# Kernel tuning notes

Measured on AMD Instinct MI355X. Metric: run time of the kernel, lower is better.

The kernel has to match this reference:

```python
import jax, jax.numpy as jnp
import numpy as np

B, S, IN, H, NC, WSEG = 2, 256, 80, 128, 40, 64
F2 = 2 * H  # bidirectional LSTM output dim


def setup_inputs() -> dict:
    key = jax.random.key(0)
    it = iter(jax.random.split(key, 48))
    def nrm(shape, scale):
        return jax.random.normal(next(it), shape, jnp.float32) * scale
    d = {}
    d["x"] = jax.random.normal(next(it), (B, S, IN), jnp.float32)
    d["lengths"] = jnp.full((B,), S, dtype=jnp.int32)
    ins = [IN, F2]
    for l in range(2):
        for dr in ("f", "b"):
            sc = 1.0 / np.sqrt(H)
            d[f"w_ih_l{l}{dr}"] = nrm((4 * H, ins[l]), sc)
            d[f"w_hh_l{l}{dr}"] = nrm((4 * H, H), sc)
            d[f"b_l{l}{dr}"] = nrm((4 * H,), sc)
    PD = 3 * F2  # pairwise phi feature dim
    d["a_s0"] = jnp.float32(0.25); d["w_s1"] = nrm((100, PD), 1.0 / np.sqrt(PD)); d["b_s1"] = jnp.zeros((100,), jnp.float32)
    d["a_s1"] = jnp.float32(0.25); d["w_s2"] = nrm((1, 100), 0.1); d["b_s2"] = jnp.zeros((1,), jnp.float32)
    d["a_c0"] = jnp.float32(0.25); d["w_c1"] = nrm((2 * NC, F2), 1.0 / np.sqrt(F2)); d["b_c1"] = jnp.zeros((2 * NC,), jnp.float32)
    d["a_c1"] = jnp.float32(0.25); d["w_c2"] = nrm((NC, 2 * NC), 0.1); d["b_c2"] = jnp.zeros((NC,), jnp.float32)
    d["a_b0"] = jnp.float32(0.25); d["w_b1"] = nrm((2 * NC, F2), 1.0 / np.sqrt(F2)); d["b_b1"] = jnp.zeros((2 * NC,), jnp.float32)
    d["a_b1"] = jnp.float32(0.25); d["w_b2"] = nrm((2, 2 * NC), 0.1); d["b_b2"] = jnp.zeros((2,), jnp.float32)
    return d


def prelu(x, a):
    return jnp.where(x >= 0, x, a * x)


def mlp(x, a0, W1, b1, a1, W2, b2):
    h = prelu(x, a0) @ W1.T + b1
    return prelu(h, a1) @ W2.T + b2


def lstm_dir(x, Wih, Whh, b, reverse):
    # PyTorch gate order: i, f, g, o
    pre = jnp.einsum("bsi,gi->sbg", x, Wih) + b  # [S,B,4H]
    if reverse:
        pre = pre[::-1]
    h0 = jnp.zeros((x.shape[0], Whh.shape[1]), x.dtype)
    def step(carry, xt):
        h, c = carry
        g = xt + h @ Whh.T
        i, f, gg, o = jnp.split(g, 4, axis=-1)
        c = jax.nn.sigmoid(f) * c + jax.nn.sigmoid(i) * jnp.tanh(gg)
        h = jax.nn.sigmoid(o) * jnp.tanh(c)
        return (h, c), h
    _, hs = jax.lax.scan(step, (h0, h0), pre)
    if reverse:
        hs = hs[::-1]
    return jnp.swapaxes(hs, 0, 1)  # [B,S,H]


def encode(x, layers):
    out = x
    for (wif, whf, bf, wib, whb, bb) in layers:
        out = jnp.concatenate([
            lstm_dir(out, wif, whf, bf, False),
            lstm_dir(out, wib, whb, bb, True),
        ], axis=-1)
    return out


def compute_scores(rnn_out, a_s0, w_s1, b_s1, a_s1, w_s2, b_s2):
    cum = jnp.cumsum(rnn_out, axis=1)
    # phi[b,i,j] = [cum[j]-cum[i], out[i], out[j]]  (faithful to calc_phi)
    c = cum[:, None, :, :] - cum[:, :, None, :]
    sh = c.shape
    dmat = jnp.broadcast_to(rnn_out[:, :, None, :], sh)
    emat = jnp.broadcast_to(rnn_out[:, None, :, :], sh)
    phi = jnp.concatenate([c, dmat, emat], axis=-1)  # [B,S,S,3*F2]
    return mlp(phi, a_s0, w_s1, b_s1, a_s1, w_s2, b_s2)[..., 0]  # [B,S,S]


def dp_backptr(scores):
    # Viterbi-style DP: best[i] = max_{j in [i-WSEG, i)} best[j] + scores[:, j, i]
    Bn, Sn = scores.shape[:2]
    def step(best, i):
        start = jnp.maximum(0, i - WSEG)
        jidx = start + jnp.arange(WSEG)
        bwin = jax.lax.dynamic_slice(best, (0, start), (Bn, WSEG))
        swin = jax.lax.dynamic_slice(scores, (0, start, i), (Bn, WSEG, 1))[..., 0]
        cand = jnp.where(jidx[None, :] < i, bwin + swin, -1e9)
        k = (start + jnp.argmax(cand, axis=1)).astype(jnp.int32)
        best = jax.lax.dynamic_update_slice(best, jnp.max(cand, axis=1, keepdims=True), (0, i))
        return best, k
    _, ks = jax.lax.scan(step, jnp.zeros((Bn, Sn), scores.dtype), jnp.arange(1, Sn))
    backptr = jnp.concatenate([jnp.zeros((1, Bn), jnp.int32), ks], axis=0).T  # [B,S]
    return backptr


def backtrack(scores, backptr, lengths):
    Bn, Sn = scores.shape[:2]
    bar = jnp.arange(Bn)
    def step(carry, _):
        cur, acc, bm = carry
        bm = bm.at[bar, cur].set(True)
        prev = backptr[bar, cur]
        active = cur > 0
        acc = acc + jnp.where(active, scores[bar, prev, cur], 0.0)
        cur = jnp.where(active, prev, 0)
        return (cur, acc, bm), None
    init = ((lengths - 1).astype(jnp.int32), jnp.zeros((Bn,), scores.dtype), jnp.zeros((Bn, Sn), bool))
    (_, acc, bm), _ = jax.lax.scan(step, init, None, length=Sn)
    return bm, acc


def reference(x, lengths,
              w_ih_l0f, w_hh_l0f, b_l0f, w_ih_l0b, w_hh_l0b, b_l0b,
              w_ih_l1f, w_hh_l1f, b_l1f, w_ih_l1b, w_hh_l1b, b_l1b,
              a_s0, w_s1, b_s1, a_s1, w_s2, b_s2,
              a_c0, w_c1, b_c1, a_c1, w_c2, b_c2,
              a_b0, w_b1, b_b1, a_b1, w_b2, b_b2):
    layers = [
        (w_ih_l0f, w_hh_l0f, b_l0f, w_ih_l0b, w_hh_l0b, b_l0b),
        (w_ih_l1f, w_hh_l1f, b_l1f, w_ih_l1b, w_hh_l1b, b_l1b),
    ]
    rnn_out = encode(x, layers)  # [B,S,2H]
    cls_out = mlp(rnn_out, a_c0, w_c1, b_c1, a_c1, w_c2, b_c2)
    bin_out = mlp(rnn_out, a_b0, w_b1, b_b1, a_b1, w_b2, b_b2)
    scores = compute_scores(rnn_out, a_s0, w_s1, b_s1, a_s1, w_s2, b_s2)
    backptr = dp_backptr(scores)
    bmask, pred_scores = backtrack(scores, backptr, lengths)
    # bmask[b,i]==1 iff i is a predicted segment boundary (padded-dense encoding of pred lists)
    return cls_out, bin_out, bmask.astype(jnp.int32), pred_scores
```

## Files before the change

kernel.cpp:

```cpp
#include <hip/hip_runtime.h>
#include <math.h>


#define OFF_BIN 20480
#define OFF_BM  21504
#define OFF_PRED 22016

__device__ __forceinline__ float preluf(float x, float a) { return x >= 0.f ? x : a * x; }
__device__ __forceinline__ float sigf(float x) { return 1.f / (1.f + __expf(-x)); }
__device__ __forceinline__ float tanh_fast(float x) { return 1.f - 2.f / (__expf(2.f * x) + 1.f); }

__global__ __launch_bounds__(256) void k_gemm(const float* __restrict__ A,
                                              const float* __restrict__ B,
                                              int Adim, int K,
                                              const float* __restrict__ wf,
                                              const float* __restrict__ bf,
                                              const float* __restrict__ wb,
                                              const float* __restrict__ bbv,
                                              float* __restrict__ outF,
                                              float* __restrict__ outB) {
    int mtile = blockIdx.y;
    int dir = mtile >> 3;
    const float* W = dir ? wb : wf;
    const float* bias = dir ? bbv : bf;
    float* out = dir ? outB : outF;
    int g0 = (mtile & 7) << 6;
    int tb0 = blockIdx.x << 6;
    int tid = threadIdx.x;
    int Bdim = K - Adim;

    __shared__ float Ws[16][68];
    __shared__ float Xs[16][68];

    int r = tid >> 2, c4 = tid & 3;
    int tbr = tb0 + r;
    int hr = ((tbr & 1) << 8) | (tbr >> 1);
    int ty = tid >> 4;
    int tx = tid & 15;
    float acc[4][4] = {};

    for (int k0 = 0; k0 < K; k0 += 16) {
        float4 wv = *(const float4*)(W + (size_t)(g0 + r) * K + k0 + (c4 << 2));
        const float* src = (k0 < Adim) ? (A + (size_t)hr * Adim + k0)
                                       : (B + (size_t)hr * Bdim + (k0 - Adim));
        float4 xv = *(const float4*)(src + (c4 << 2));
        __syncthreads();
        int kc = c4 << 2;
        Ws[kc + 0][r] = wv.x; Ws[kc + 1][r] = wv.y; Ws[kc + 2][r] = wv.z; Ws[kc + 3][r] = wv.w;
        Xs[kc + 0][r] = xv.x; Xs[kc + 1][r] = xv.y; Xs[kc + 2][r] = xv.z; Xs[kc + 3][r] = xv.w;
        __syncthreads();
#pragma unroll
        for (int kk = 0; kk < 16; ++kk) {
            float4 wq = *(const float4*)&Ws[kk][ty << 2];
            float4 xq = *(const float4*)&Xs[kk][tx << 2];
            acc[0][0] += wq.x * xq.x; acc[0][1] += wq.x * xq.y; acc[0][2] += wq.x * xq.z; acc[0][3] += wq.x * xq.w;
            acc[1][0] += wq.y * xq.x; acc[1][1] += wq.y * xq.y; acc[1][2] += wq.y * xq.z; acc[1][3] += wq.y * xq.w;
            acc[2][0] += wq.z * xq.x; acc[2][1] += wq.z * xq.y; acc[2][2] += wq.z * xq.z; acc[2][3] += wq.z * xq.w;
            acc[3][0] += wq.w * xq.x; acc[3][1] += wq.w * xq.y; acc[3][2] += wq.w * xq.z; acc[3][3] += wq.w * xq.w;
        }
    }
    int gq = g0 + (ty << 2);
    float b0 = bias[gq], b1 = bias[gq + 1], b2 = bias[gq + 2], b3 = bias[gq + 3];
#pragma unroll
    for (int j = 0; j < 4; ++j) {
        int tb = tb0 + (tx << 2) + j;
        float4 v = make_float4(acc[0][j] + b0, acc[1][j] + b1, acc[2][j] + b2, acc[3][j] + b3);
        *(float4*)(out + (size_t)tb * 512 + gq) = v;
    }
}

__global__ __launch_bounds__(512, 2) void k_lstm(const float* __restrict__ pre_f,
                                                 const float* __restrict__ pre_b,
                                                 const float* __restrict__ whh_f,
                                                 const float* __restrict__ whh_b,
                                                 float* __restrict__ hout_f,
                                                 float* __restrict__ hout_b) {
    const int dir = blockIdx.x >> 1;
    const int b = blockIdx.x & 1;
    const float* pre = dir ? pre_b : pre_f;
    const float* whh = dir ? whh_b : whh_f;
    float* hout = dir ? hout_b : hout_f;
    const int tid = threadIdx.x;
    const int c = tid >> 7;
    const int gg = tid & 127;
    const int k0 = c << 5;

    float w[4][32];
#pragma unroll
    for (int j = 0; j < 4; ++j) {
#pragma unroll
        for (int k = 0; k < 32; k += 4) {
            float4 v = *(const float4*)(whh + (size_t)((j << 7) + gg) * 128 + k0 + k);
            w[j][k] = v.x; w[j][k + 1] = v.y; w[j][k + 2] = v.z; w[j][k + 3] = v.w;
        }
    }

    __shared__ __align__(16) float hl[128];
    __shared__ float4 part[4][128];
    if (tid < 128) hl[tid] = 0.f;
    float cst = 0.f;
    __syncthreads();

    int t0 = dir ? 255 : 0;
    const float* pp0 = pre + ((size_t)t0 * 2 + b) * 512;
    float p0 = pp0[gg], p1 = pp0[128 + gg], p2 = pp0[256 + gg], p3 = pp0[384 + gg];

    for (int step = 0; step < 256; ++step) {
        int t = dir ? (255 - step) : step;
        float n0 = 0.f, n1 = 0.f, n2 = 0.f, n3 = 0.f;
        if (step < 255) {
            int tn = dir ? (254 - step) : (step + 1);
            const float* pp = pre + ((size_t)tn * 2 + b) * 512;
            n0 = pp[gg]; n1 = pp[128 + gg]; n2 = pp[256 + gg]; n3 = pp[384 + gg];
        }
        float a0 = 0.f, a1 = 0.f, a2 = 0.f, a3 = 0.f;
#pragma unroll
        for (int k = 0; k < 32; k += 4) {
            float4 h4 = *(const float4*)(hl + k0 + k);
            a0 += w[0][k] * h4.x + w[0][k + 1] * h4.y + w[0][k + 2] * h4.z + w[0][k + 3] * h4.w;
            a1 += w[1][k] * h4.x + w[1][k + 1] * h4.y + w[1][k + 2] * h4.z + w[1][k + 3] * h4.w;
            a2 += w[2][k] * h4.x + w[2][k + 1] * h4.y + w[2][k + 2] * h4.z + w[2][k + 3] * h4.w;
            a3 += w[3][k] * h4.x + w[3][k + 1] * h4.y + w[3][k + 2] * h4.z + w[3][k + 3] * h4.w;
        }
        part[c][gg] = make_float4(a0, a1, a2, a3);
        __syncthreads();
        float4 q0 = part[0][gg], q1 = part[1][gg], q2 = part[2][gg], q3 = part[3][gg];
        float gi = p0 + ((q0.x + q1.x) + (q2.x + q3.x));
        float gf = p1 + ((q0.y + q1.y) + (q2.y + q3.y));
        float gG = p2 + ((q0.z + q1.z) + (q2.z + q3.z));
        float go = p3 + ((q0.w + q1.w) + (q2.w + q3.w));
        cst = sigf(gf) * cst + sigf(gi) * tanh_fast(gG);
        float h = sigf(go) * tanh_fast(cst);
        hl[gg] = h;
        if (tid < 128) hout[(size_t)(((b << 8) + t) << 7) + gg] = h;
        p0 = n0; p1 = n1; p2 = n2; p3 = n3;
        __syncthreads();
    }
}

__global__ __launch_bounds__(256) void k_feats(const float* __restrict__ h1f,
                                               const float* __restrict__ h1b,
                                               const float* __restrict__ ws1,
                                               const float* __restrict__ bs1,
                                               const float* a_s0,
                                               float* __restrict__ Pd,
                                               float* __restrict__ Pe,
                                               const float* ac0p, const float* __restrict__ wc1,
                                               const float* __restrict__ bc1, const float* ac1p,
                                               const float* __restrict__ wc2, const float* __restrict__ bc2,
                                               const float* ab0p, const float* __restrict__ wb1,
                                               const float* __restrict__ bb1, const float* ab1p,
                                               const float* __restrict__ wb2, const float* __restrict__ bb2,
                                               float* __restrict__ out,
                                               float* __restrict__ cum) {
    __shared__ __align__(16) float xa[256];
    __shared__ __align__(16) float xb2[256];
    __shared__ __align__(16) float hc[80];
    __shared__ __align__(16) float hb[80];
    int bid = blockIdx.x;
    int tid = threadIdx.x;
    int kk = tid & 127;
    if (bid < 512) {
        int row = bid;
        float a0 = a_s0[0];
        float v = ((tid < 128) ? h1f : h1b)[(size_t)row * 128 + kk];
        xa[tid] = preluf(v, a0);
        __syncthreads();
        const float4* p4 = (const float4*)xa;
        if (tid < 100) {
            const float4* wr = (const float4*)(ws1 + (size_t)tid * 768 + 256);
            float acc = bs1[tid];
#pragma unroll 8
            for (int q = 0; q < 64; ++q) {
                float4 w4 = wr[q], x4 = p4[q];
                acc += w4.x * x4.x + w4.y * x4.y + w4.z * x4.z + w4.w * x4.w;
            }
            Pd[(size_t)row * 100 + tid] = acc;
        } else if (tid >= 128 && tid < 228) {
            int u = tid - 128;
            const float4* wr = (const float4*)(ws1 + (size_t)u * 768 + 512);
            float acc = 0.f;
#pragma unroll 8
            for (int q = 0; q < 64; ++q) {
                float4 w4 = wr[q], x4 = p4[q];
                acc += w4.x * x4.x + w4.y * x4.y + w4.z * x4.z + w4.w * x4.w;
            }
            Pe[(size_t)row * 100 + u] = acc;
        }
    } else if (bid < 1024) {
        int row = bid - 512;
        float ac0 = ac0p[0], ac1 = ac1p[0], ab0 = ab0p[0], ab1 = ab1p[0];
        float v = ((tid < 128) ? h1f : h1b)[(size_t)row * 128 + kk];
        xa[tid] = preluf(v, ac0);
        xb2[tid] = preluf(v, ab0);
        __syncthreads();
        if (tid < 80) {
            const float4* wr = (const float4*)(wc1 + (size_t)tid * 256);
            const float4* x4 = (const float4*)xa;
            float acc = bc1[tid];
#pragma unroll 8
            for (int q = 0; q < 64; ++q) {
                float4 w4 = wr[q], p = x4[q];
                acc += w4.x * p.x + w4.y * p.y + w4.z * p.z + w4.w * p.w;
            }
            hc[tid] = preluf(acc, ac1);
        } else if (tid >= 128 && tid < 208) {
            int u = tid - 128;
            const float4* wr = (const float4*)(wb1 + (size_t)u * 256);
            const float4* x4 = (const float4*)xb2;
            float acc = bb1[u];
#pragma unroll 8
            for (int q = 0; q < 64; ++q) {
                float4 w4 = wr[q], p = x4[q];
                acc += w4.x * p.x + w4.y * p.y + w4.z * p.z + w4.w * p.w;
            }
            hb[u] = preluf(acc, ab1);
        }
        __syncthreads();
        if (tid < 40) {
            const float4* wr = (const float4*)(wc2 + (size_t)tid * 80);
            const float4* h4 = (const float4*)hc;
            float acc = bc2[tid];
#pragma unroll
            for (int q = 0; q < 20; ++q) {
                float4 w4 = wr[q], p = h4[q];
                acc += w4.x * p.x + w4.y * p.y + w4.z * p.z + w4.w * p.w;
            }
            out[(size_t)row * 40 + tid] = acc;
        } else if (tid >= 64 && tid < 66) {
            int j = tid - 64;
            const float4* wr = (const float4*)(wb2 + (size_t)j * 80);
            const float4* h4 = (const float4*)hb;
            float acc = bb2[j];
#pragma unroll
            for (int q = 0; q < 20; ++q) {
                float4 w4 = wr[q], p = h4[q];
                acc += w4.x * p.x + w4.y * p.y + w4.z * p.z + w4.w * p.w;
            }
            out[OFF_BIN + (size_t)row * 2 + j] = acc;
        }
    } else {
        int b = bid - 1024;
        const float* src = (tid < 128) ? h1f : h1b;
        float run = 0.f;
#pragma unroll 8
        for (int t = 0; t < 256; ++t) {
            float v = src[(size_t)(((b << 8) + t) << 7) + kk];
            cum[(size_t)(((b << 8) + t) << 8) + tid] = run + v;
            run += v;
        }
    }
}

__global__ __launch_bounds__(256, 4) void k_scores(const float* __restrict__ cum,
                                                   const float* __restrict__ ws1,
                                                   const float* __restrict__ ws2,
                                                   const float* __restrict__ bs2,
                                                   const float* __restrict__ Pd,
                                                   const float* __restrict__ Pe,
                                                   const float* a_s0p, const float* a_s1p,
                                                   float* __restrict__ scT) {
    int bid = blockIdx.x;
    int dt = bid & 7, et = (bid >> 3) & 63, b = bid >> 9;
    int d0 = dt << 5, e0 = et << 2;
    int tid = threadIdx.x;
    __shared__ float cumd[32][257];
    __shared__ float cume[4][257];
    __shared__ float red[4][4][32];
    float a0 = a_s0p[0], a1 = a_s1p[0];

    {
        int r = tid & 31, w = tid >> 5;
        const float4* src = (const float4*)(cum + (size_t)(((b << 8) + (d0 + r)) << 8) + (w << 5));
        float* dst = &cumd[r][w << 5];
#pragma unroll
        for (int x = 0; x < 8; ++x) {
            float4 v = src[x];
            dst[(x << 2) + 0] = v.x; dst[(x << 2) + 1] = v.y;
            dst[(x << 2) + 2] = v.z; dst[(x << 2) + 3] = v.w;
        }
    }
    {
        int er = tid >> 6, j = tid & 63;
        float4 v = *((const float4*)(cum + (size_t)(((b << 8) + (e0 + er)) << 8)) + j);
        float* dst = &cume[er][j << 2];
        dst[0] = v.x; dst[1] = v.y; dst[2] = v.z; dst[3] = v.w;
    }
    __syncthreads();

    int ug = __builtin_amdgcn_readfirstlane(tid >> 6);
    int lane = tid & 63;
    int dd = lane & 31;
    int eh = lane >> 5;
    int ea = (eh << 1), ebn = ea + 1;
    float acc0[25], acc1[25];
#pragma unroll
    for (int t = 0; t < 25; ++t) { acc0[t] = 0.f; acc1[t] = 0.f; }
    const float* wc = ws1 + (size_t)(ug * 25) * 768;

    for (int k = 0; k < 256; k += 4) {
        float cd0 = cumd[dd][k], cd1 = cumd[dd][k + 1], cd2 = cumd[dd][k + 2], cd3 = cumd[dd][k + 3];
        float4 ya = make_float4(preluf(cume[ea][k] - cd0, a0), preluf(cume[ea][k + 1] - cd1, a0),
                                preluf(cume[ea][k + 2] - cd2, a0), preluf(cume[ea][k + 3] - cd3, a0));
        float4 yb = make_float4(preluf(cume[ebn][k] - cd0, a0), preluf(cume[ebn][k + 1] - cd1, a0),
                                preluf(cume[ebn][k + 2] - cd2, a0), preluf(cume[ebn][k + 3] - cd3, a0));
#pragma unroll
        for (int t = 0; t < 25; ++t) {
            float4 wq = *(const float4*)(wc + (size_t)t * 768 + k);
            acc0[t] += ya.x * wq.x + ya.y * wq.y + ya.z * wq.z + ya.w * wq.w;
            acc1[t] += yb.x * wq.x + yb.y * wq.y + yb.z * wq.z + yb.w * wq.w;
        }
    }

    const float* pdrow = Pd + (size_t)((b << 8) + d0 + dd) * 100;
    {
        const float* perow = Pe + (size_t)((b << 8) + e0 + ea) * 100;
        float part = 0.f;
#pragma unroll
        for (int t = 0; t < 25; ++t) {
            int u = ug * 25 + t;
            float h = acc0[t] + pdrow[u] + perow[u];
            part += preluf(h, a1) * ws2[u];
        }
        red[ug][ea][dd] = part;
    }
    {
        const float* perow = Pe + (size_t)((b << 8) + e0 + ebn) * 100;
        float part = 0.f;
#pragma unroll
        for (int t = 0; t < 25; ++t) {
            int u = ug * 25 + t;
            float h = acc1[t] + pdrow[u] + perow[u];
            part += preluf(h, a1) * ws2[u];
        }
        red[ug][ebn][dd] = part;
    }
    __syncthreads();
    if (tid < 128) {
        int e = tid >> 5, l2 = tid & 31;
        float s = red[0][e][l2] + red[1][e][l2] + red[2][e][l2] + red[3][e][l2] + bs2[0];
        scT[(size_t)(((b << 8) + (e0 + e)) << 8) + d0 + l2] = s;
    }
}

__device__ __forceinline__ void argmax_dpp(float& v, int& ki) {
#define AD_STEP(CTRL, RMASK)                                                                    \
    {                                                                                           \
        int mv = __builtin_amdgcn_update_dpp(__float_as_int(v), __float_as_int(v), CTRL, RMASK, 0xf, false); \
        int mk = __builtin_amdgcn_update_dpp(ki, ki, CTRL, RMASK, 0xf, false);                  \
        float fv = __int_as_float(mv);                                                          \
        bool take = (fv > v) || (fv == v && mk < ki);                                           \
        v = take ? fv : v;                                                                      \
        ki = take ? mk : ki;                                                                    \
    }
    AD_STEP(0x111, 0xf)
    AD_STEP(0x112, 0xf)
    AD_STEP(0x114, 0xf)
    AD_STEP(0x118, 0xf)
    AD_STEP(0x142, 0xa)
    AD_STEP(0x143, 0xc)
#undef AD_STEP
}

__global__ __launch_bounds__(128) void k_dp(const float* __restrict__ scT,
                                            const int* __restrict__ lengths,
                                            float* __restrict__ out) {
    __shared__ int bp[2][256];
    __shared__ float bm[2][256];
    int tid = threadIdx.x;
    for (int i = tid; i < 512; i += 128) {
        ((int*)bp)[i] = 0;
        ((float*)bm)[i] = 0.f;
    }
    __syncthreads();
    int b = tid >> 6, ln = tid & 63;
    const float* sb = scT + ((size_t)b << 16);
    int lenm1 = lengths[b] - 1;
    float wreg = 0.f;
    float bestFinal = 0.f;
    int jcur = (ln < 1) ? ln : ln - 64;
    float sc_next = sb[(1 << 8) + ((jcur < 0) ? 0 : jcur)];
    for (int i = 1; i < 256; ++i) {
        float sc = sc_next;
        int j = jcur;
        if (i < 255) {
            int m2 = (i + 1) & 63;
            int base2 = (i + 1) - m2;
            int j2 = (ln < m2) ? (base2 + ln) : (base2 + ln - 64);
            jcur = j2;
            sc_next = sb[((i + 1) << 8) + ((j2 < 0) ? 0 : j2)];
        }
        float v = (j >= 0) ? (wreg + sc) : -1000000000.0f;
        int ki = j;
        argmax_dpp(v, ki);
        float bv = __uint_as_float(__builtin_amdgcn_readlane(__float_as_uint(v), 63));
        int bk = __builtin_amdgcn_readlane(ki, 63);
        if (ln == (i & 63)) wreg = bv;
        if (ln == 0) bp[b][i] = bk;
        if (i == lenm1) bestFinal = bv;
    }
    if (ln == 0) out[OFF_PRED + b] = bestFinal;
    __syncthreads();
    if (tid < 2) {
        int bb = tid;
        int cur = lengths[bb] - 1;
        for (int it = 0; it < 256; ++it) {
            bm[bb][cur] = 1.f;
            int prev = bp[bb][cur];
            cur = (cur > 0) ? prev : 0;
        }
    }
    __syncthreads();
    for (int i = tid; i < 512; i += 128) out[OFF_BM + i] = ((float*)bm)[i];
}

extern "C" void kernel_launch(void* const* d_in, const int* in_sizes, int n_in,
                              void* d_out, int out_size, void* d_ws, size_t ws_size,
                              hipStream_t stream) {
    const float* x     = (const float*)d_in[0];
    const int* lengths = (const int*)d_in[1];
    const float* wih0f = (const float*)d_in[2];
    const float* whh0f = (const float*)d_in[3];
    const float* b0f   = (const float*)d_in[4];
    const float* wih0b = (const float*)d_in[5];
    const float* whh0b = (const float*)d_in[6];
    const float* b0b   = (const float*)d_in[7];
    const float* wih1f = (const float*)d_in[8];
    const float* whh1f = (const float*)d_in[9];
    const float* b1f   = (const float*)d_in[10];
    const float* wih1b = (const float*)d_in[11];
    const float* whh1b = (const float*)d_in[12];
    const float* b1b   = (const float*)d_in[13];
    const float* a_s0  = (const float*)d_in[14];
    const float* w_s1  = (const float*)d_in[15];
    const float* b_s1  = (const float*)d_in[16];
    const float* a_s1  = (const float*)d_in[17];
    const float* w_s2  = (const float*)d_in[18];
    const float* b_s2  = (const float*)d_in[19];
    const float* a_c0  = (const float*)d_in[20];
    const float* w_c1  = (const float*)d_in[21];
    const float* b_c1  = (const float*)d_in[22];
    const float* a_c1  = (const float*)d_in[23];
    const float* w_c2  = (const float*)d_in[24];
    const float* b_c2  = (const float*)d_in[25];
    const float* a_b0  = (const float*)d_in[26];
    const float* w_b1  = (const float*)d_in[27];
    const float* b_b1  = (const float*)d_in[28];
    const float* a_b1  = (const float*)d_in[29];
    const float* w_b2  = (const float*)d_in[30];
    const float* b_b2  = (const float*)d_in[31];

    float* wsf = (float*)d_ws;
    float* preF = wsf;
    float* preB = wsf + 262144;
    float* h0f  = wsf + 524288;
    float* h0b  = wsf + 589824;
    float* h1f  = wsf + 655360;
    float* h1b  = wsf + 720896;
    float* cum  = wsf + 786432;
    float* Pd   = wsf + 917504;
    float* Pe   = wsf + 968704;
    float* scT  = wsf + 1019904;
    float* out  = (float*)d_out;

    k_gemm<<<dim3(8, 16), 256, 0, stream>>>(x, x, 80, 80, wih0f, b0f, wih0b, b0b, preF, preB);
    k_lstm<<<4, 512, 0, stream>>>(preF, preB, whh0f, whh0b, h0f, h0b);
    k_gemm<<<dim3(8, 16), 256, 0, stream>>>(h0f, h0b, 128, 256, wih1f, b1f, wih1b, b1b, preF, preB);
    k_lstm<<<4, 512, 0, stream>>>(preF, preB, whh1f, whh1b, h1f, h1b);
    k_feats<<<1026, 256, 0, stream>>>(h1f, h1b, w_s1, b_s1, a_s0, Pd, Pe,
                                      a_c0, w_c1, b_c1, a_c1, w_c2, b_c2,
                                      a_b0, w_b1, b_b1, a_b1, w_b2, b_b2, out, cum);
    k_scores<<<1024, 256, 0, stream>>>(cum, w_s1, w_s2, b_s2, Pd, Pe, a_s0, a_s1, scT);
    k_dp<<<1, 128, 0, stream>>>(scT, lengths, out);
}
```

Baseline: 957.5 us.

## Batch LSTM preactivation loads and output stores; retile pairwise scores kernel

The LSTM recurrence now loads pre-activations for eight timesteps at once and buffers eight hidden outputs before writing them. This takes a global load off the serial per-step critical path. The dot product is split into two accumulator chains to shorten the dependency. The scores kernel is retiled to 512-thread blocks covering 64 d-rows and 4 e-rows, staging the cumulative sums in two K-halves so shared memory stays small while each weight load is reused across more rows. The costs are extra register pressure in both kernels, fewer blocks in the scores launch, and an extra barrier per K-half.

```diff
diff --git a/kernel.cpp b/kernel.cpp
--- a/kernel.cpp
+++ b/kernel.cpp
@@ -99,42 +99,60 @@
     __shared__ float4 part[4][128];
     if (tid < 128) hl[tid] = 0.f;
     float cst = 0.f;
+    float pf0[8], pf1[8], pf2[8], pf3[8], hb8[8];
     __syncthreads();
 
-    int t0 = dir ? 255 : 0;
-    const float* pp0 = pre + ((size_t)t0 * 2 + b) * 512;
-    float p0 = pp0[gg], p1 = pp0[128 + gg], p2 = pp0[256 + gg], p3 = pp0[384 + gg];
-
-    for (int step = 0; step < 256; ++step) {
-        int t = dir ? (255 - step) : step;
-        float n0 = 0.f, n1 = 0.f, n2 = 0.f, n3 = 0.f;
-        if (step < 255) {
-            int tn = dir ? (254 - step) : (step + 1);
-            const float* pp = pre + ((size_t)tn * 2 + b) * 512;
-            n0 = pp[gg]; n1 = pp[128 + gg]; n2 = pp[256 + gg]; n3 = pp[384 + gg];
-        }
-        float a0 = 0.f, a1 = 0.f, a2 = 0.f, a3 = 0.f;
-#pragma unroll
-        for (int k = 0; k < 32; k += 4) {
-            float4 h4 = *(const float4*)(hl + k0 + k);
-            a0 += w[0][k] * h4.x + w[0][k + 1] * h4.y + w[0][k + 2] * h4.z + w[0][k + 3] * h4.w;
-            a1 += w[1][k] * h4.x + w[1][k + 1] * h4.y + w[1][k + 2] * h4.z + w[1][k + 3] * h4.w;
-            a2 += w[2][k] * h4.x + w[2][k + 1] * h4.y + w[2][k + 2] * h4.z + w[2][k + 3] * h4.w;
-            a3 += w[3][k] * h4.x + w[3][k + 1] * h4.y + w[3][k + 2] * h4.z + w[3][k + 3] * h4.w;
-        }
-        part[c][gg] = make_float4(a0, a1, a2, a3);
-        __syncthreads();
-        float4 q0 = part[0][gg], q1 = part[1][gg], q2 = part[2][gg], q3 = part[3][gg];
-        float gi = p0 + ((q0.x + q1.x) + (q2.x + q3.x));
-        float gf = p1 + ((q0.y + q1.y) + (q2.y + q3.y));
-        float gG = p2 + ((q0.z + q1.z) + (q2.z + q3.z));
-        float go = p3 + ((q0.w + q1.w) + (q2.w + q3.w));
-        cst = sigf(gf) * cst + sigf(gi) * tanh_fast(gG);
-        float h = sigf(go) * tanh_fast(cst);
-        hl[gg] = h;
-        if (tid < 128) hout[(size_t)(((b << 8) + t) << 7) + gg] = h;
-        p0 = n0; p1 = n1; p2 = n2; p3 = n3;
-        __syncthreads();
+    for (int blk = 0; blk < 32; ++blk) {
+        if (tid < 128) {
+#pragma unroll
+            for (int s = 0; s < 8; ++s) {
+                int step = (blk << 3) + s;
+                int t = dir ? (255 - step) : step;
+                const float* pp = pre + ((size_t)t * 2 + b) * 512;
+                pf0[s] = pp[gg]; pf1[s] = pp[128 + gg];
+                pf2[s] = pp[256 + gg]; pf3[s] = pp[384 + gg];
+            }
+        }
+#pragma unroll
+        for (int s = 0; s < 8; ++s) {
+            float a0 = 0.f, a1 = 0.f, a2 = 0.f, a3 = 0.f;
+            float e0 = 0.f, e1 = 0.f, e2 = 0.f, e3 = 0.f;
+#pragma unroll
+            for (int k = 0; k < 32; k += 8) {
+                float4 hA = *(const float4*)(hl + k0 + k);
+                float4 hB = *(const float4*)(hl + k0 + k + 4);
+                a0 += w[0][k] * hA.x + w[0][k + 1] * hA.y + w[0][k + 2] * hA.z + w[0][k + 3] * hA.w;
+                e0 += w[0][k + 4] * hB.x + w[0][k + 5] * hB.y + w[0][k + 6] * hB.z + w[0][k + 7] * hB.w;
+                a1 += w[1][k] * hA.x + w[1][k + 1] * hA.y + w[1][k + 2] * hA.z + w[1][k + 3] * hA.w;
+                e1 += w[1][k + 4] * hB.x + w[1][k + 5] * hB.y + w[1][k + 6] * hB.z + w[1][k + 7] * hB.w;
+                a2 += w[2][k] * hA.x + w[2][k + 1] * hA.y + w[2][k + 2] * hA.z + w[2][k + 3] * hA.w;
+                e2 += w[2][k + 4] * hB.x + w[2][k + 5] * hB.y + w[2][k + 6] * hB.z + w[2][k + 7] * hB.w;
+                a3 += w[3][k] * hA.x + w[3][k + 1] * hA.y + w[3][k + 2] * hA.z + w[3][k + 3] * hA.w;
+                e3 += w[3][k + 4] * hB.x + w[3][k + 5] * hB.y + w[3][k + 6] * hB.z + w[3][k + 7] * hB.w;
+            }
+            part[c][gg] = make_float4(a0 + e0, a1 + e1, a2 + e2, a3 + e3);
+            __syncthreads();
+            if (tid < 128) {
+                float4 q0 = part[0][gg], q1 = part[1][gg], q2 = part[2][gg], q3 = part[3][gg];
+                float gi = pf0[s] + ((q0.x + q1.x) + (q2.x + q3.x));
+                float gf = pf1[s] + ((q0.y + q1.y) + (q2.y + q3.y));
+                float gG = pf2[s] + ((q0.z + q1.z) + (q2.z + q3.z));
+                float go = pf3[s] + ((q0.w + q1.w) + (q2.w + q3.w));
+                cst = sigf(gf) * cst + sigf(gi) * tanh_fast(gG);
+                float h = sigf(go) * tanh_fast(cst);
+                hl[gg] = h;
+                hb8[s] = h;
+            }
+            __syncthreads();
+        }
+        if (tid < 128) {
+            int base = blk << 3;
+#pragma unroll
+            for (int s = 0; s < 8; ++s) {
+                int t = dir ? (255 - (base + s)) : (base + s);
+                hout[(size_t)(((b << 8) + t) << 7) + gg] = hb8[s];
+            }
+        }
     }
 }
 
@@ -252,7 +270,7 @@
     }
 }
 
-__global__ __launch_bounds__(256, 4) void k_scores(const float* __restrict__ cum,
+__global__ __launch_bounds__(512, 2) void k_scores(const float* __restrict__ cum,
                                                    const float* __restrict__ ws1,
                                                    const float* __restrict__ ws2,
                                                    const float* __restrict__ bs2,
@@ -261,54 +279,59 @@
                                                    const float* a_s0p, const float* a_s1p,
                                                    float* __restrict__ scT) {
     int bid = blockIdx.x;
-    int dt = bid & 7, et = (bid >> 3) & 63, b = bid >> 9;
-    int d0 = dt << 5, e0 = et << 2;
+    int dt = bid & 3, et = (bid >> 2) & 63, b = bid >> 8;
+    int d0 = dt << 6, e0 = et << 2;
     int tid = threadIdx.x;
-    __shared__ float cumd[32][257];
-    __shared__ float cume[4][257];
-    __shared__ float red[4][4][32];
+    __shared__ float cumdh[64][129];
+    __shared__ float cumeh[4][129];
+    __shared__ float red[4][4][64];
     float a0 = a_s0p[0], a1 = a_s1p[0];
 
-    {
-        int r = tid & 31, w = tid >> 5;
-        const float4* src = (const float4*)(cum + (size_t)(((b << 8) + (d0 + r)) << 8) + (w << 5));
-        float* dst = &cumd[r][w << 5];
-#pragma unroll
-        for (int x = 0; x < 8; ++x) {
-            float4 v = src[x];
-            dst[(x << 2) + 0] = v.x; dst[(x << 2) + 1] = v.y;
-            dst[(x << 2) + 2] = v.z; dst[(x << 2) + 3] = v.w;
-        }
-    }
-    {
-        int er = tid >> 6, j = tid & 63;
-        float4 v = *((const float4*)(cum + (size_t)(((b << 8) + (e0 + er)) << 8)) + j);
-        float* dst = &cume[er][j << 2];
-        dst[0] = v.x; dst[1] = v.y; dst[2] = v.z; dst[3] = v.w;
-    }
-    __syncthreads();
-
-    int ug = __builtin_amdgcn_readfirstlane(tid >> 6);
-    int lane = tid & 63;
-    int dd = lane & 31;
-    int eh = lane >> 5;
-    int ea = (eh << 1), ebn = ea + 1;
+    int wv = tid >> 6;
+    int ug = __builtin_amdgcn_readfirstlane(wv & 3);
+    int eh = __builtin_amdgcn_readfirstlane(wv >> 2);
+    int dd = tid & 63;
+    int ea = eh << 1, ebn = ea + 1;
     float acc0[25], acc1[25];
 #pragma unroll
     for (int t = 0; t < 25; ++t) { acc0[t] = 0.f; acc1[t] = 0.f; }
     const float* wc = ws1 + (size_t)(ug * 25) * 768;
 
-    for (int k = 0; k < 256; k += 4) {
-        float cd0 = cumd[dd][k], cd1 = cumd[dd][k + 1], cd2 = cumd[dd][k + 2], cd3 = cumd[dd][k + 3];
-        float4 ya = make_float4(preluf(cume[ea][k] - cd0, a0), preluf(cume[ea][k + 1] - cd1, a0),
-                                preluf(cume[ea][k + 2] - cd2, a0), preluf(cume[ea][k + 3] - cd3, a0));
-        float4 yb = make_float4(preluf(cume[ebn][k] - cd0, a0), preluf(cume[ebn][k + 1] - cd1, a0),
-                                preluf(cume[ebn][k + 2] - cd2, a0), preluf(cume[ebn][k + 3] - cd3, a0));
-#pragma unroll
-        for (int t = 0; t < 25; ++t) {
-            float4 wq = *(const float4*)(wc + (size_t)t * 768 + k);
-            acc0[t] += ya.x * wq.x + ya.y * wq.y + ya.z * wq.z + ya.w * wq.w;
-            acc1[t] += yb.x * wq.x + yb.y * wq.y + yb.z * wq.z + yb.w * wq.w;
+    for (int half = 0; half < 2; ++half) {
+        int hk = half << 7;
+        __syncthreads();
+        {
+            int r = tid & 63, wq = tid >> 6;
+            const float4* src = (const float4*)(cum + (size_t)(((b << 8) + (d0 + r)) << 8) + hk + (wq << 4));
+            float* dst = &cumdh[r][wq << 4];
+#pragma unroll
+            for (int x = 0; x < 4; ++x) {
+                float4 v = src[x];
+                dst[(x << 2) + 0] = v.x; dst[(x << 2) + 1] = v.y;
+                dst[(x << 2) + 2] = v.z; dst[(x << 2) + 3] = v.w;
+            }
+        }
+        if (tid < 128) {
+            int er = tid >> 5, j = tid & 31;
+            float4 v = *((const float4*)(cum + (size_t)(((b << 8) + (e0 + er)) << 8) + hk) + j);
+            float* dst = &cumeh[er][j << 2];
+            dst[0] = v.x; dst[1] = v.y; dst[2] = v.z; dst[3] = v.w;
+        }
+        __syncthreads();
+
+        for (int k = 0; k < 128; k += 4) {
+            float cd0 = cumdh[dd][k], cd1 = cumdh[dd][k + 1],
+                  cd2 = cumdh[dd][k + 2], cd3 = cumdh[dd][k + 3];
+            float4 ya = make_float4(preluf(cumeh[ea][k] - cd0, a0), preluf(cumeh[ea][k + 1] - cd1, a0),
+                                    preluf(cumeh[ea][k + 2] - cd2, a0), preluf(cumeh[ea][k + 3] - cd3, a0));
+            float4 yb = make_float4(preluf(cumeh[ebn][k] - cd0, a0), preluf(cumeh[ebn][k + 1] - cd1, a0),
+                                    preluf(cumeh[ebn][k + 2] - cd2, a0), preluf(cumeh[ebn][k + 3] - cd3, a0));
+#pragma unroll
+            for (int t = 0; t < 25; ++t) {
+                float4 wq = *(const float4*)(wc + (size_t)t * 768 + hk + k);
+                acc0[t] += ya.x * wq.x + ya.y * wq.y + ya.z * wq.z + ya.w * wq.w;
+                acc1[t] += yb.x * wq.x + yb.y * wq.y + yb.z * wq.z + yb.w * wq.w;
+            }
         }
     }
 
@@ -336,8 +359,8 @@
         red[ug][ebn][dd] = part;
     }
     __syncthreads();
-    if (tid < 128) {
-        int e = tid >> 5, l2 = tid & 31;
+    if (tid < 256) {
+        int e = tid >> 6, l2 = tid & 63;
         float s = red[0][e][l2] + red[1][e][l2] + red[2][e][l2] + red[3][e][l2] + bs2[0];
         scT[(size_t)(((b << 8) + (e0 + e)) << 8) + d0 + l2] = s;
     }
@@ -470,6 +493,6 @@
     k_feats<<<1026, 256, 0, stream>>>(h1f, h1b, w_s1, b_s1, a_s0, Pd, Pe,
                                       a_c0, w_c1, b_c1, a_c1, w_c2, b_c2,
                                       a_b0, w_b1, b_b1, a_b1, w_b2, b_b2, out, cum);
-    k_scores<<<1024, 256, 0, stream>>>(cum, w_s1, w_s2, b_s2, Pd, Pe, a_s0, a_s1, scT);
+    k_scores<<<512, 512, 0, stream>>>(cum, w_s1, w_s2, b_s2, Pd, Pe, a_s0, a_s1, scT);
     k_dp<<<1, 128, 0, stream>>>(scT, lengths, out);
 }
```

Measured after the change: 984.0 us. 2.8% more time.
